# Performance work log

Hardware: AMD Instinct MI355X
Metric: run time of the kernel (lower is better)

## Reference

```python
import jax, jax.numpy as jnp
import numpy as np

B, T, H, D = 1, 2048, 32, 64
SCALE = 0.015625  # 1/64 = 1/head_size
DEG = 2


def setup_inputs() -> dict:
    key = jax.random.key(0)
    k1, k2, k3, k4 = jax.random.split(key, 4)
    q = jax.random.normal(k1, (B, T, H, D), dtype=jnp.float32)
    k = jax.random.normal(k2, (B, T, H, D), dtype=jnp.float32)
    v = jax.random.normal(k3, (B, T, H, D), dtype=jnp.float32)
    # log_G: per-token, per-head log decay (must be <= 0)
    g = -0.1 * jax.random.uniform(k4, (B, T, H), dtype=jnp.float32)
    return {"q": q, "k": k, "v": v, "g": g}


def reference(q, k, v, g):
    # q,k,v: [B,T,H,D]; g: [B,T,H] log-decay (log_G)
    # Power retention, deg=2, attention (quadratic) form for T <= switch_over_seq_len.
    g_cum = jnp.cumsum(g, axis=1)                         # [B,T,H]
    gc = jnp.transpose(g_cum, (0, 2, 1))                  # [B,H,T]
    # decay weight exp(gc[t]-gc[s]) for s<=t, 0 otherwise
    log_decay = gc[:, :, :, None] - gc[:, :, None, :]     # [B,H,T,S]
    causal = jnp.tril(jnp.ones((T, T), dtype=bool))
    decay = jnp.where(causal, jnp.exp(log_decay), 0.0)    # [B,H,T,S]
    qk = jnp.einsum("bthd,bshd->bhts", q, k) * SCALE      # [B,H,T,S]
    w = (qk ** DEG) * decay                               # nonneg scores, deg=2
    num = jnp.einsum("bhts,bshd->bthd", w, v)             # [B,T,H,D]
    denom = jnp.transpose(w.sum(-1), (0, 2, 1))           # [B,T,H]
    out = num / jnp.maximum(denom, 1.0)[..., None]
    return out
```

## Files before the change

### kernel.cpp

```cpp
#include <hip/hip_runtime.h>

#define T_DIM 2048
#define H_DIM 32
#define D_DIM 64
#define SCALE_F 0.015625f
#define NPAIR 32
#define TILE_STRIDE 2048

typedef unsigned short ushort;
typedef __attribute__((ext_vector_type(8))) short short8;
typedef __attribute__((ext_vector_type(16))) float f32x16;

__global__ __launch_bounds__(256)
void cumsum_g_kernel(const float* __restrict__ g, float* __restrict__ gc) {
    const int h = blockIdx.x;
    const int tid = threadIdx.x;
    const int PER = T_DIM / 256;

    __shared__ float sums[256];

    float loc[8];
    float run = 0.f;
    const int t0 = tid * PER;
    for (int i = 0; i < PER; ++i) {
        run += g[(size_t)(t0 + i) * H_DIM + h];
        loc[i] = run;
    }
    sums[tid] = run;
    __syncthreads();

    for (int off = 1; off < 256; off <<= 1) {
        float vv = (tid >= off) ? sums[tid - off] : 0.f;
        __syncthreads();
        sums[tid] += vv;
        __syncthreads();
    }
    float excl = (tid == 0) ? 0.f : sums[tid - 1];

    for (int i = 0; i < PER; ++i)
        gc[(size_t)h * T_DIM + t0 + i] = excl + loc[i];
}

__device__ __forceinline__ ushort f2bf(float x) {
    unsigned u = __float_as_uint(x);
    unsigned r = (u + 0x7fffu + ((u >> 16) & 1u)) >> 16;
    return (ushort)r;
}

__global__ __launch_bounds__(256)
void prep_kernel(const float* __restrict__ q, const float* __restrict__ k,
                 const float* __restrict__ v, const float* __restrict__ gc,
                 ushort* __restrict__ qfrag, ushort* __restrict__ kfrag,
                 ushort* __restrict__ vfrag) {
    __shared__ ushort qt_l[64 * 64];
    __shared__ ushort kt_l[64 * 64];

    const int tt  = blockIdx.x;
    const int h   = blockIdx.y;
    const int tid = threadIdx.x;

    {
        const int r    = tid >> 2;
        const int dseg = (tid & 3) * 16;
        const int t    = tt * 64 + r;
        const float gct = gc[(size_t)h * T_DIM + t];
        const float eq = SCALE_F * __expf(0.5f * gct);
        const float ek = __expf(-0.5f * gct);
        const float* qp = q + ((size_t)t * H_DIM + h) * 64 + dseg;
        const float* kp = k + ((size_t)t * H_DIM + h) * 64 + dseg;
        union { ushort u[16]; uint4 uu[2]; } oq, ok;
#pragma unroll
        for (int i = 0; i < 16; ++i) {
            oq.u[i] = f2bf(qp[i] * eq);
            ok.u[i] = f2bf(kp[i] * ek);
        }
        const int c0 = (tid & 3) * 2;
#pragma unroll
        for (int cc = 0; cc < 2; ++cc) {
            const int slot = (c0 + cc) ^ (r & 7);
            *reinterpret_cast<uint4*>(&qt_l[r * 64 + slot * 8]) = oq.uu[cc];
            *reinterpret_cast<uint4*>(&kt_l[r * 64 + slot * 8]) = ok.uu[cc];
        }
    }
    __syncthreads();

#pragma unroll
    for (int n = 0; n < 2; ++n) {
        const int ch   = tid + 256 * n;
        const int l31  = ch & 31;
        const int hi   = (ch >> 5) & 1;
        const int ks   = (ch >> 6) & 3;
        const int t32r = ch >> 8;
        const int row  = t32r * 32 + l31;
        const int slot = (2 * ks + hi) ^ (row & 7);
        uint4 qq = *reinterpret_cast<const uint4*>(&qt_l[row * 64 + slot * 8]);
        uint4 kk = *reinterpret_cast<const uint4*>(&kt_l[row * 64 + slot * 8]);
        const size_t base = ((size_t)h * 64 + tt * 2 + t32r) * TILE_STRIDE
                          + (size_t)(((ks * 2 + hi) * 32) + l31) * 8;
        *reinterpret_cast<uint4*>(qfrag + base) = qq;
        *reinterpret_cast<uint4*>(kfrag + base) = kk;
    }

#pragma unroll
    for (int n = 0; n < 2; ++n) {
        const int c9   = (tid >> 5) + 8 * n;
        const int l31  = tid & 31;
        const int hi   = c9 & 1;
        const int kh2  = (c9 >> 1) & 1;
        const int dblk = (c9 >> 2) & 1;
        const int s32r = c9 >> 3;
        const int tb = tt * 64 + s32r * 32 + kh2 * 16 + hi * 8;
        union { ushort u[8]; uint4 uu; } ov;
#pragma unroll
        for (int j = 0; j < 8; ++j)
            ov.u[j] = f2bf(v[((size_t)(tb + j) * H_DIM + h) * 64 + dblk * 32 + l31]);
        const size_t base = ((size_t)h * 64 + tt * 2 + s32r) * TILE_STRIDE
                          + (size_t)((((dblk * 2 + kh2) * 2 + hi) * 32) + l31) * 8;
        *reinterpret_cast<uint4*>(vfrag + base) = ov.uu;
    }
}

__device__ __forceinline__ short8 ld8(const ushort* p) {
    return *reinterpret_cast<const short8*>(p);
}

__device__ __forceinline__ unsigned cvt_pk_bf16(float lo, float hi) {
    unsigned r;
    asm("v_cvt_pk_bf16_f32 %0, %1, %2" : "=v"(r) : "v"(lo), "v"(hi));
    return r;
}

template<bool DIAG>
__device__ __forceinline__ void step32(
    const ushort* __restrict__ kb, const ushort* __restrict__ vb,
    int lofs, int hi, int l31,
    const short8 (&qr)[4], f32x16& o0, f32x16& o1, float& den)
{
    const short8 vf00 = ld8(vb + lofs);
    const short8 vf10 = ld8(vb + 512 + lofs);
    const short8 vf01 = ld8(vb + 1024 + lofs);
    const short8 vf11 = ld8(vb + 1536 + lofs);
    const short8 kf0 = ld8(kb + lofs);
    const short8 kf1 = ld8(kb + 512 + lofs);
    const short8 kf2 = ld8(kb + 1024 + lofs);
    const short8 kf3 = ld8(kb + 1536 + lofs);

    f32x16 c;
#pragma unroll
    for (int i = 0; i < 16; ++i) c[i] = 0.f;
    c = __builtin_amdgcn_mfma_f32_32x32x16_bf16(kf0, qr[0], c, 0, 0, 0);
    c = __builtin_amdgcn_mfma_f32_32x32x16_bf16(kf1, qr[1], c, 0, 0, 0);
    c = __builtin_amdgcn_mfma_f32_32x32x16_bf16(kf2, qr[2], c, 0, 0, 0);
    c = __builtin_amdgcn_mfma_f32_32x32x16_bf16(kf3, qr[3], c, 0, 0, 0);

    float w[16];
#pragma unroll
    for (int r = 0; r < 16; ++r) {
        float x = c[r];
        float ww = x * x;
        if (DIAG) {
            const int s_local = (r & 3) + 8 * (r >> 2) + 4 * hi;
            ww = (s_local <= l31) ? ww : 0.f;
        }
        w[r] = ww;
        den += ww;
    }

#pragma unroll
    for (int kh2 = 0; kh2 < 2; ++kh2) {
        const int b = 8 * kh2;
        unsigned p0 = cvt_pk_bf16(w[b + 0], w[b + 1]);
        unsigned p1 = cvt_pk_bf16(w[b + 2], w[b + 3]);
        unsigned p2 = cvt_pk_bf16(w[b + 4], w[b + 5]);
        unsigned p3 = cvt_pk_bf16(w[b + 6], w[b + 7]);
        asm("v_permlane32_swap_b32 %0, %1" : "+v"(p0), "+v"(p2));
        asm("v_permlane32_swap_b32 %0, %1" : "+v"(p1), "+v"(p3));
        union { unsigned u[4]; short8 s; } af;
        af.u[0] = p0; af.u[1] = p1; af.u[2] = p2; af.u[3] = p3;
        if (kh2 == 0) {
            o0 = __builtin_amdgcn_mfma_f32_32x32x16_bf16(af.s, vf00, o0, 0, 0, 0);
            o1 = __builtin_amdgcn_mfma_f32_32x32x16_bf16(af.s, vf01, o1, 0, 0, 0);
        } else {
            o0 = __builtin_amdgcn_mfma_f32_32x32x16_bf16(af.s, vf10, o0, 0, 0, 0);
            o1 = __builtin_amdgcn_mfma_f32_32x32x16_bf16(af.s, vf11, o1, 0, 0, 0);
        }
    }
}

__device__ __forceinline__ void process_subtile(
    int oo, int h, int w, int hi, int l31, int lofs,
    const ushort* __restrict__ qfrag, const ushort* __restrict__ kfrag,
    const ushort* __restrict__ vfrag, float* __restrict__ out,
    float* lds_o, float* lds_den)
{
    short8 qr[4];
    const ushort* qb = qfrag + ((size_t)h * 64 + oo) * TILE_STRIDE;
#pragma unroll
    for (int ks = 0; ks < 4; ++ks) qr[ks] = ld8(qb + ks * 512 + lofs);

    f32x16 o0, o1;
#pragma unroll
    for (int i = 0; i < 16; ++i) { o0[i] = 0.f; o1[i] = 0.f; }
    float den = 0.f;

    const ushort* kh_b = kfrag + (size_t)h * 64 * TILE_STRIDE;
    const ushort* vh_b = vfrag + (size_t)h * 64 * TILE_STRIDE;

    for (int st = w; st < oo; st += 4)
        step32<false>(kh_b + (size_t)st * TILE_STRIDE, vh_b + (size_t)st * TILE_STRIDE,
                      lofs, hi, l31, qr, o0, o1, den);
    if ((oo & 3) == w)
        step32<true>(kh_b + (size_t)oo * TILE_STRIDE, vh_b + (size_t)oo * TILE_STRIDE,
                     lofs, hi, l31, qr, o0, o1, den);

    den += __shfl_xor(den, 32);

    __syncthreads();
#pragma unroll
    for (int r = 0; r < 16; ++r) {
        const int row = (r & 3) + 8 * (r >> 2) + 4 * hi;
        lds_o[((w * 2 + 0) * 32 + row) * 32 + l31] = o0[r];
        lds_o[((w * 2 + 1) * 32 + row) * 32 + l31] = o1[r];
    }
    if (hi == 0) lds_den[w * 32 + l31] = den;
    __syncthreads();

    const float dtot = lds_den[l31] + lds_den[32 + l31] +
                       lds_den[64 + l31] + lds_den[96 + l31];
    const int t0 = oo * 32;
#pragma unroll
    for (int qq = 0; qq < 4; ++qq) {
        const int row = qq + 8 * w + 4 * hi;
        float s0 = 0.f, s1 = 0.f;
#pragma unroll
        for (int ww = 0; ww < 4; ++ww) {
            s0 += lds_o[((ww * 2 + 0) * 32 + row) * 32 + l31];
            s1 += lds_o[((ww * 2 + 1) * 32 + row) * 32 + l31];
        }
        const float dt = __shfl(dtot, row);
        const float inv = 1.f / fmaxf(dt, 1.f);
        float* op = out + ((size_t)(t0 + row) * H_DIM + h) * 64;
        op[l31]      = s0 * inv;
        op[32 + l31] = s1 * inv;
    }
}

__global__ __launch_bounds__(256, 4)
void retention_mfma_kernel(const ushort* __restrict__ qfrag,
                           const ushort* __restrict__ kfrag,
                           const ushort* __restrict__ vfrag,
                           float* __restrict__ out) {
    __shared__ float lds_o[4 * 2 * 32 * 32];
    __shared__ float lds_den[4 * 32];

    const int bid = blockIdx.x;
    const int p   = bid >> 5;
    const int h   = bid & 31;
    const int lane = threadIdx.x & 63;
    const int w    = threadIdx.x >> 6;
    const int hi   = lane >> 5;
    const int l31  = lane & 31;
    const int lofs = hi * 256 + l31 * 8;

    process_subtile(63 - p, h, w, hi, l31, lofs, qfrag, kfrag, vfrag, out, lds_o, lds_den);
    process_subtile(p,      h, w, hi, l31, lofs, qfrag, kfrag, vfrag, out, lds_o, lds_den);
}

extern "C" void kernel_launch(void* const* d_in, const int* in_sizes, int n_in,
                              void* d_out, int out_size, void* d_ws, size_t ws_size,
                              hipStream_t stream) {
    const float* q = (const float*)d_in[0];
    const float* k = (const float*)d_in[1];
    const float* v = (const float*)d_in[2];
    const float* g = (const float*)d_in[3];
    float* out = (float*)d_out;

    const size_t GC_BYTES = (size_t)H_DIM * T_DIM * sizeof(float);
    const size_t BF_ELEMS = (size_t)H_DIM * T_DIM * D_DIM;

    float* gc = (float*)d_ws;
    ushort* qfrag = (ushort*)((char*)d_ws + GC_BYTES);
    ushort* kfrag = qfrag + BF_ELEMS;
    ushort* vfrag = kfrag + BF_ELEMS;

    cumsum_g_kernel<<<H_DIM, 256, 0, stream>>>(g, gc);
    prep_kernel<<<dim3(T_DIM / 64, H_DIM), 256, 0, stream>>>(q, k, v, gc,
                                                             qfrag, kfrag, vfrag);
    retention_mfma_kernel<<<NPAIR * H_DIM, 256, 0, stream>>>(qfrag, kfrag, vfrag, out);
}
```

Before: 47.88 us.

## Process 64-row query tiles per block to reuse K/V fragment loads

```diff
diff --git a/kernel.cpp b/kernel.cpp
--- a/kernel.cpp
+++ b/kernel.cpp
@@ -4,7 +4,6 @@
 #define H_DIM 32
 #define D_DIM 64
 #define SCALE_F 0.015625f
-#define NPAIR 32
 #define TILE_STRIDE 2048
 
 typedef unsigned short ushort;
@@ -55,8 +54,8 @@
     __shared__ ushort qt_l[64 * 64];
     __shared__ ushort kt_l[64 * 64];
 
-    const int tt  = blockIdx.x;
-    const int h   = blockIdx.y;
+    const int h   = blockIdx.x;
+    const int tt  = blockIdx.y;
     const int tid = threadIdx.x;
 
     {
@@ -130,11 +129,25 @@
     return r;
 }
 
-template<bool DIAG>
-__device__ __forceinline__ void step32(
+__device__ __forceinline__ short8 pack_w(const float* w8) {
+    unsigned p0 = cvt_pk_bf16(w8[0], w8[1]);
+    unsigned p1 = cvt_pk_bf16(w8[2], w8[3]);
+    unsigned p2 = cvt_pk_bf16(w8[4], w8[5]);
+    unsigned p3 = cvt_pk_bf16(w8[6], w8[7]);
+    asm("v_permlane32_swap_b32 %0, %1" : "+v"(p0), "+v"(p2));
+    asm("v_permlane32_swap_b32 %0, %1" : "+v"(p1), "+v"(p3));
+    union { unsigned u[4]; short8 s; } af;
+    af.u[0] = p0; af.u[1] = p1; af.u[2] = p2; af.u[3] = p3;
+    return af.s;
+}
+
+template<int MODE>
+__device__ __forceinline__ void step64(
     const ushort* __restrict__ kb, const ushort* __restrict__ vb,
     int lofs, int hi, int l31,
-    const short8 (&qr)[4], f32x16& o0, f32x16& o1, float& den)
+    const short8 (&qrL)[4], const short8 (&qrH)[4],
+    f32x16& o00, f32x16& o01, f32x16& o10, f32x16& o11,
+    float& denL, float& denH)
 {
     const short8 vf00 = ld8(vb + lofs);
     const short8 vf10 = ld8(vb + 512 + lofs);
@@ -145,113 +158,145 @@
     const short8 kf2 = ld8(kb + 1024 + lofs);
     const short8 kf3 = ld8(kb + 1536 + lofs);
 
-    f32x16 c;
-#pragma unroll
-    for (int i = 0; i < 16; ++i) c[i] = 0.f;
-    c = __builtin_amdgcn_mfma_f32_32x32x16_bf16(kf0, qr[0], c, 0, 0, 0);
-    c = __builtin_amdgcn_mfma_f32_32x32x16_bf16(kf1, qr[1], c, 0, 0, 0);
-    c = __builtin_amdgcn_mfma_f32_32x32x16_bf16(kf2, qr[2], c, 0, 0, 0);
-    c = __builtin_amdgcn_mfma_f32_32x32x16_bf16(kf3, qr[3], c, 0, 0, 0);
-
-    float w[16];
+    f32x16 cH;
+#pragma unroll
+    for (int i = 0; i < 16; ++i) cH[i] = 0.f;
+    f32x16 cL = cH;
+
+    if (MODE <= 1) {
+        cL = __builtin_amdgcn_mfma_f32_32x32x16_bf16(kf0, qrL[0], cL, 0, 0, 0);
+        cH = __builtin_amdgcn_mfma_f32_32x32x16_bf16(kf0, qrH[0], cH, 0, 0, 0);
+        cL = __builtin_amdgcn_mfma_f32_32x32x16_bf16(kf1, qrL[1], cL, 0, 0, 0);
+        cH = __builtin_amdgcn_mfma_f32_32x32x16_bf16(kf1, qrH[1], cH, 0, 0, 0);
+        cL = __builtin_amdgcn_mfma_f32_32x32x16_bf16(kf2, qrL[2], cL, 0, 0, 0);
+        cH = __builtin_amdgcn_mfma_f32_32x32x16_bf16(kf2, qrH[2], cH, 0, 0, 0);
+        cL = __builtin_amdgcn_mfma_f32_32x32x16_bf16(kf3, qrL[3], cL, 0, 0, 0);
+        cH = __builtin_amdgcn_mfma_f32_32x32x16_bf16(kf3, qrH[3], cH, 0, 0, 0);
+    } else {
+        cH = __builtin_amdgcn_mfma_f32_32x32x16_bf16(kf0, qrH[0], cH, 0, 0, 0);
+        cH = __builtin_amdgcn_mfma_f32_32x32x16_bf16(kf1, qrH[1], cH, 0, 0, 0);
+        cH = __builtin_amdgcn_mfma_f32_32x32x16_bf16(kf2, qrH[2], cH, 0, 0, 0);
+        cH = __builtin_amdgcn_mfma_f32_32x32x16_bf16(kf3, qrH[3], cH, 0, 0, 0);
+    }
+
+    float wL[16], wH[16];
 #pragma unroll
     for (int r = 0; r < 16; ++r) {
-        float x = c[r];
-        float ww = x * x;
-        if (DIAG) {
-            const int s_local = (r & 3) + 8 * (r >> 2) + 4 * hi;
-            ww = (s_local <= l31) ? ww : 0.f;
+        const int s_local = (r & 3) + 8 * (r >> 2) + 4 * hi;
+        float xh = cH[r];
+        float wwh = xh * xh;
+        if (MODE == 2) wwh = (s_local <= l31) ? wwh : 0.f;
+        wH[r] = wwh;
+        denH += wwh;
+        if (MODE <= 1) {
+            float xl = cL[r];
+            float wwl = xl * xl;
+            if (MODE == 1) wwl = (s_local <= l31) ? wwl : 0.f;
+            wL[r] = wwl;
+            denL += wwl;
         }
-        w[r] = ww;
-        den += ww;
-    }
-
-#pragma unroll
-    for (int kh2 = 0; kh2 < 2; ++kh2) {
-        const int b = 8 * kh2;
-        unsigned p0 = cvt_pk_bf16(w[b + 0], w[b + 1]);
-        unsigned p1 = cvt_pk_bf16(w[b + 2], w[b + 3]);
-        unsigned p2 = cvt_pk_bf16(w[b + 4], w[b + 5]);
-        unsigned p3 = cvt_pk_bf16(w[b + 6], w[b + 7]);
-        asm("v_permlane32_swap_b32 %0, %1" : "+v"(p0), "+v"(p2));
-        asm("v_permlane32_swap_b32 %0, %1" : "+v"(p1), "+v"(p3));
-        union { unsigned u[4]; short8 s; } af;
-        af.u[0] = p0; af.u[1] = p1; af.u[2] = p2; af.u[3] = p3;
-        if (kh2 == 0) {
-            o0 = __builtin_amdgcn_mfma_f32_32x32x16_bf16(af.s, vf00, o0, 0, 0, 0);
-            o1 = __builtin_amdgcn_mfma_f32_32x32x16_bf16(af.s, vf01, o1, 0, 0, 0);
-        } else {
-            o0 = __builtin_amdgcn_mfma_f32_32x32x16_bf16(af.s, vf10, o0, 0, 0, 0);
-            o1 = __builtin_amdgcn_mfma_f32_32x32x16_bf16(af.s, vf11, o1, 0, 0, 0);
-        }
-    }
-}
-
-__device__ __forceinline__ void process_subtile(
-    int oo, int h, int w, int hi, int l31, int lofs,
+    }
+
+    if (MODE <= 1) {
+        const short8 a0 = pack_w(&wL[0]);
+        o00 = __builtin_amdgcn_mfma_f32_32x32x16_bf16(a0, vf00, o00, 0, 0, 0);
+        o01 = __builtin_amdgcn_mfma_f32_32x32x16_bf16(a0, vf01, o01, 0, 0, 0);
+        const short8 a1 = pack_w(&wL[8]);
+        o00 = __builtin_amdgcn_mfma_f32_32x32x16_bf16(a1, vf10, o00, 0, 0, 0);
+        o01 = __builtin_amdgcn_mfma_f32_32x32x16_bf16(a1, vf11, o01, 0, 0, 0);
+    }
+    {
+        const short8 a0 = pack_w(&wH[0]);
+        o10 = __builtin_amdgcn_mfma_f32_32x32x16_bf16(a0, vf00, o10, 0, 0, 0);
+        o11 = __builtin_amdgcn_mfma_f32_32x32x16_bf16(a0, vf01, o11, 0, 0, 0);
+        const short8 a1 = pack_w(&wH[8]);
+        o10 = __builtin_amdgcn_mfma_f32_32x32x16_bf16(a1, vf10, o10, 0, 0, 0);
+        o11 = __builtin_amdgcn_mfma_f32_32x32x16_bf16(a1, vf11, o11, 0, 0, 0);
+    }
+}
+
+__device__ __forceinline__ void epi_phase(
+    int thalf, const f32x16& od0, const f32x16& od1,
+    int t0, int h, int w, int hi, int l31,
+    float* __restrict__ out, float* lds_o, const float* lds_den)
+{
+    __syncthreads();
+#pragma unroll
+    for (int r = 0; r < 16; ++r) {
+        const int row = (r & 3) + 8 * (r >> 2) + 4 * hi;
+        lds_o[((w * 2 + 0) * 32 + row) * 32 + l31] = od0[r];
+        lds_o[((w * 2 + 1) * 32 + row) * 32 + l31] = od1[r];
+    }
+    __syncthreads();
+#pragma unroll
+    for (int rr = 0; rr < 8; ++rr) {
+        const int row = 8 * w + rr;
+        const float s = lds_o[((0 + hi) * 32 + row) * 32 + l31]
+                      + lds_o[((2 + hi) * 32 + row) * 32 + l31]
+                      + lds_o[((4 + hi) * 32 + row) * 32 + l31]
+                      + lds_o[((6 + hi) * 32 + row) * 32 + l31];
+        const float dt = lds_den[(0 + thalf) * 32 + row]
+                       + lds_den[(2 + thalf) * 32 + row]
+                       + lds_den[(4 + thalf) * 32 + row]
+                       + lds_den[(6 + thalf) * 32 + row];
+        const float inv = 1.f / fmaxf(dt, 1.f);
+        out[((size_t)(t0 + thalf * 32 + row) * H_DIM + h) * 64 + hi * 32 + l31]
+            = s * inv;
+    }
+}
+
+__device__ __forceinline__ void process_tile64(
+    int tt, int h, int w, int hi, int l31, int lofs,
     const ushort* __restrict__ qfrag, const ushort* __restrict__ kfrag,
     const ushort* __restrict__ vfrag, float* __restrict__ out,
     float* lds_o, float* lds_den)
 {
-    short8 qr[4];
-    const ushort* qb = qfrag + ((size_t)h * 64 + oo) * TILE_STRIDE;
-#pragma unroll
-    for (int ks = 0; ks < 4; ++ks) qr[ks] = ld8(qb + ks * 512 + lofs);
-
-    f32x16 o0, o1;
-#pragma unroll
-    for (int i = 0; i < 16; ++i) { o0[i] = 0.f; o1[i] = 0.f; }
-    float den = 0.f;
+    short8 qrL[4], qrH[4];
+    const ushort* qb = qfrag + ((size_t)h * 64 + 2 * tt) * TILE_STRIDE;
+#pragma unroll
+    for (int ks = 0; ks < 4; ++ks) {
+        qrL[ks] = ld8(qb + ks * 512 + lofs);
+        qrH[ks] = ld8(qb + TILE_STRIDE + ks * 512 + lofs);
+    }
+
+    f32x16 o00, o01, o10, o11;
+#pragma unroll
+    for (int i = 0; i < 16; ++i) { o00[i] = 0.f; o01[i] = 0.f; o10[i] = 0.f; o11[i] = 0.f; }
+    float denL = 0.f, denH = 0.f;
 
     const ushort* kh_b = kfrag + (size_t)h * 64 * TILE_STRIDE;
     const ushort* vh_b = vfrag + (size_t)h * 64 * TILE_STRIDE;
-
-    for (int st = w; st < oo; st += 4)
-        step32<false>(kh_b + (size_t)st * TILE_STRIDE, vh_b + (size_t)st * TILE_STRIDE,
-                      lofs, hi, l31, qr, o0, o1, den);
-    if ((oo & 3) == w)
-        step32<true>(kh_b + (size_t)oo * TILE_STRIDE, vh_b + (size_t)oo * TILE_STRIDE,
-                     lofs, hi, l31, qr, o0, o1, den);
-
-    den += __shfl_xor(den, 32);
-
-    __syncthreads();
-#pragma unroll
-    for (int r = 0; r < 16; ++r) {
-        const int row = (r & 3) + 8 * (r >> 2) + 4 * hi;
-        lds_o[((w * 2 + 0) * 32 + row) * 32 + l31] = o0[r];
-        lds_o[((w * 2 + 1) * 32 + row) * 32 + l31] = o1[r];
-    }
-    if (hi == 0) lds_den[w * 32 + l31] = den;
-    __syncthreads();
-
-    const float dtot = lds_den[l31] + lds_den[32 + l31] +
-                       lds_den[64 + l31] + lds_den[96 + l31];
-    const int t0 = oo * 32;
-#pragma unroll
-    for (int qq = 0; qq < 4; ++qq) {
-        const int row = qq + 8 * w + 4 * hi;
-        float s0 = 0.f, s1 = 0.f;
-#pragma unroll
-        for (int ww = 0; ww < 4; ++ww) {
-            s0 += lds_o[((ww * 2 + 0) * 32 + row) * 32 + l31];
-            s1 += lds_o[((ww * 2 + 1) * 32 + row) * 32 + l31];
-        }
-        const float dt = __shfl(dtot, row);
-        const float inv = 1.f / fmaxf(dt, 1.f);
-        float* op = out + ((size_t)(t0 + row) * H_DIM + h) * 64;
-        op[l31]      = s0 * inv;
-        op[32 + l31] = s1 * inv;
-    }
-}
-
-__global__ __launch_bounds__(256, 4)
+    const int dlo = 2 * tt;
+
+    for (int st = w; st < dlo; st += 4)
+        step64<0>(kh_b + (size_t)st * TILE_STRIDE, vh_b + (size_t)st * TILE_STRIDE,
+                  lofs, hi, l31, qrL, qrH, o00, o01, o10, o11, denL, denH);
+    if ((dlo & 3) == w)
+        step64<1>(kh_b + (size_t)dlo * TILE_STRIDE, vh_b + (size_t)dlo * TILE_STRIDE,
+                  lofs, hi, l31, qrL, qrH, o00, o01, o10, o11, denL, denH);
+    if (((dlo + 1) & 3) == w)
+        step64<2>(kh_b + (size_t)(dlo + 1) * TILE_STRIDE, vh_b + (size_t)(dlo + 1) * TILE_STRIDE,
+                  lofs, hi, l31, qrL, qrH, o00, o01, o10, o11, denL, denH);
+
+    denL += __shfl_xor(denL, 32);
+    denH += __shfl_xor(denH, 32);
+    if (hi == 0) {
+        lds_den[(w * 2 + 0) * 32 + l31] = denL;
+        lds_den[(w * 2 + 1) * 32 + l31] = denH;
+    }
+
+    const int t0 = tt * 64;
+    epi_phase(0, o00, o01, t0, h, w, hi, l31, out, lds_o, lds_den);
+    epi_phase(1, o10, o11, t0, h, w, hi, l31, out, lds_o, lds_den);
+}
+
+__global__ __launch_bounds__(256, 2)
 void retention_mfma_kernel(const ushort* __restrict__ qfrag,
                            const ushort* __restrict__ kfrag,
                            const ushort* __restrict__ vfrag,
                            float* __restrict__ out) {
     __shared__ float lds_o[4 * 2 * 32 * 32];
-    __shared__ float lds_den[4 * 32];
+    __shared__ float lds_den[4 * 2 * 32];
 
     const int bid = blockIdx.x;
     const int p   = bid >> 5;
@@ -262,8 +307,8 @@
     const int l31  = lane & 31;
     const int lofs = hi * 256 + l31 * 8;
 
-    process_subtile(63 - p, h, w, hi, l31, lofs, qfrag, kfrag, vfrag, out, lds_o, lds_den);
-    process_subtile(p,      h, w, hi, l31, lofs, qfrag, kfrag, vfrag, out, lds_o, lds_den);
+    process_tile64(31 - p, h, w, hi, l31, lofs, qfrag, kfrag, vfrag, out, lds_o, lds_den);
+    process_tile64(p,      h, w, hi, l31, lofs, qfrag, kfrag, vfrag, out, lds_o, lds_den);
 }
 
 extern "C" void kernel_launch(void* const* d_in, const int* in_sizes, int n_in,
@@ -284,7 +329,7 @@
     ushort* vfrag = kfrag + BF_ELEMS;
 
     cumsum_g_kernel<<<H_DIM, 256, 0, stream>>>(g, gc);
-    prep_kernel<<<dim3(T_DIM / 64, H_DIM), 256, 0, stream>>>(q, k, v, gc,
+    prep_kernel<<<dim3(H_DIM, T_DIM / 64), 256, 0, stream>>>(q, k, v, gc,
                                                              qfrag, kfrag, vfrag);
-    retention_mfma_kernel<<<NPAIR * H_DIM, 256, 0, stream>>>(qfrag, kfrag, vfrag, out);
-}
+    retention_mfma_kernel<<<16 * H_DIM, 256, 0, stream>>>(qfrag, kfrag, vfrag, out);
+}
```

Result: faster. 45.47 us (-5.0%).

## Stage K/V tiles through LDS with double-buffered async loads over 64-row tile pairs

Applied to the files above, without the earlier changes.

```diff
diff --git a/kernel.cpp b/kernel.cpp
--- a/kernel.cpp
+++ b/kernel.cpp
@@ -4,12 +4,14 @@
 #define H_DIM 32
 #define D_DIM 64
 #define SCALE_F 0.015625f
-#define NPAIR 32
 #define TILE_STRIDE 2048
 
 typedef unsigned short ushort;
 typedef __attribute__((ext_vector_type(8))) short short8;
 typedef __attribute__((ext_vector_type(16))) float f32x16;
+typedef __attribute__((ext_vector_type(2))) float f32x2;
+
+#define MFMA32(A, B, C) __builtin_amdgcn_mfma_f32_32x32x16_bf16((A), (B), (C), 0, 0, 0)
 
 __global__ __launch_bounds__(256)
 void cumsum_g_kernel(const float* __restrict__ g, float* __restrict__ gc) {
@@ -55,8 +57,8 @@
     __shared__ ushort qt_l[64 * 64];
     __shared__ ushort kt_l[64 * 64];
 
-    const int tt  = blockIdx.x;
-    const int h   = blockIdx.y;
+    const int h   = blockIdx.x;
+    const int tt  = blockIdx.y;
     const int tid = threadIdx.x;
 
     {
@@ -130,140 +132,205 @@
     return r;
 }
 
-template<bool DIAG>
-__device__ __forceinline__ void step32(
-    const ushort* __restrict__ kb, const ushort* __restrict__ vb,
+__device__ __forceinline__ short8 pack_w2(const f32x2* w2) {
+    unsigned p0 = cvt_pk_bf16(w2[0][0], w2[0][1]);
+    unsigned p1 = cvt_pk_bf16(w2[1][0], w2[1][1]);
+    unsigned p2 = cvt_pk_bf16(w2[2][0], w2[2][1]);
+    unsigned p3 = cvt_pk_bf16(w2[3][0], w2[3][1]);
+    asm("v_permlane32_swap_b32 %0, %1" : "+v"(p0), "+v"(p2));
+    asm("v_permlane32_swap_b32 %0, %1" : "+v"(p1), "+v"(p3));
+    union { unsigned u[4]; short8 s; } af;
+    af.u[0] = p0; af.u[1] = p1; af.u[2] = p2; af.u[3] = p3;
+    return af.s;
+}
+
+__device__ __forceinline__ void gll16(const void* g, void* l) {
+    __builtin_amdgcn_global_load_lds(
+        (const __attribute__((address_space(1))) unsigned int*)g,
+        (__attribute__((address_space(3))) unsigned int*)l, 16, 0, 0);
+}
+
+__device__ __forceinline__ void stage16k(ushort* ldst, const char* ksrc,
+                                         const char* vsrc, int tid) {
+    char* lb = (char*)ldst + (tid >> 6) * 1024;
+    const int lo = tid * 16;
+    gll16(ksrc + lo,        lb);
+    gll16(ksrc + 4096 + lo, lb + 4096);
+    gll16(vsrc + lo,        lb + 8192);
+    gll16(vsrc + 4096 + lo, lb + 12288);
+}
+
+template<int MODE>
+__device__ __forceinline__ void unit32(
+    const ushort* ldsK, const ushort* ldsV,
     int lofs, int hi, int l31,
-    const short8 (&qr)[4], f32x16& o0, f32x16& o1, float& den)
+    const short8 (&qr)[4], f32x16& o0, f32x16& o1, f32x2& den2)
 {
-    const short8 vf00 = ld8(vb + lofs);
-    const short8 vf10 = ld8(vb + 512 + lofs);
-    const short8 vf01 = ld8(vb + 1024 + lofs);
-    const short8 vf11 = ld8(vb + 1536 + lofs);
-    const short8 kf0 = ld8(kb + lofs);
-    const short8 kf1 = ld8(kb + 512 + lofs);
-    const short8 kf2 = ld8(kb + 1024 + lofs);
-    const short8 kf3 = ld8(kb + 1536 + lofs);
+    const short8 kf0 = ld8(ldsK + lofs);
+    const short8 kf1 = ld8(ldsK + 512 + lofs);
+    const short8 kf2 = ld8(ldsK + 1024 + lofs);
+    const short8 kf3 = ld8(ldsK + 1536 + lofs);
+    const short8 vf0 = ld8(ldsV + lofs);
+    const short8 vf1 = ld8(ldsV + 512 + lofs);
+    const short8 vf2 = ld8(ldsV + 1024 + lofs);
+    const short8 vf3 = ld8(ldsV + 1536 + lofs);
 
     f32x16 c;
 #pragma unroll
     for (int i = 0; i < 16; ++i) c[i] = 0.f;
-    c = __builtin_amdgcn_mfma_f32_32x32x16_bf16(kf0, qr[0], c, 0, 0, 0);
-    c = __builtin_amdgcn_mfma_f32_32x32x16_bf16(kf1, qr[1], c, 0, 0, 0);
-    c = __builtin_amdgcn_mfma_f32_32x32x16_bf16(kf2, qr[2], c, 0, 0, 0);
-    c = __builtin_amdgcn_mfma_f32_32x32x16_bf16(kf3, qr[3], c, 0, 0, 0);
-
-    float w[16];
-#pragma unroll
-    for (int r = 0; r < 16; ++r) {
-        float x = c[r];
-        float ww = x * x;
-        if (DIAG) {
-            const int s_local = (r & 3) + 8 * (r >> 2) + 4 * hi;
-            ww = (s_local <= l31) ? ww : 0.f;
-        }
-        w[r] = ww;
-        den += ww;
-    }
-
-#pragma unroll
-    for (int kh2 = 0; kh2 < 2; ++kh2) {
-        const int b = 8 * kh2;
-        unsigned p0 = cvt_pk_bf16(w[b + 0], w[b + 1]);
-        unsigned p1 = cvt_pk_bf16(w[b + 2], w[b + 3]);
-        unsigned p2 = cvt_pk_bf16(w[b + 4], w[b + 5]);
-        unsigned p3 = cvt_pk_bf16(w[b + 6], w[b + 7]);
-        asm("v_permlane32_swap_b32 %0, %1" : "+v"(p0), "+v"(p2));
-        asm("v_permlane32_swap_b32 %0, %1" : "+v"(p1), "+v"(p3));
-        union { unsigned u[4]; short8 s; } af;
-        af.u[0] = p0; af.u[1] = p1; af.u[2] = p2; af.u[3] = p3;
-        if (kh2 == 0) {
-            o0 = __builtin_amdgcn_mfma_f32_32x32x16_bf16(af.s, vf00, o0, 0, 0, 0);
-            o1 = __builtin_amdgcn_mfma_f32_32x32x16_bf16(af.s, vf01, o1, 0, 0, 0);
-        } else {
-            o0 = __builtin_amdgcn_mfma_f32_32x32x16_bf16(af.s, vf10, o0, 0, 0, 0);
-            o1 = __builtin_amdgcn_mfma_f32_32x32x16_bf16(af.s, vf11, o1, 0, 0, 0);
-        }
-    }
-}
-
-__device__ __forceinline__ void process_subtile(
-    int oo, int h, int w, int hi, int l31, int lofs,
-    const ushort* __restrict__ qfrag, const ushort* __restrict__ kfrag,
-    const ushort* __restrict__ vfrag, float* __restrict__ out,
-    float* lds_o, float* lds_den)
-{
-    short8 qr[4];
-    const ushort* qb = qfrag + ((size_t)h * 64 + oo) * TILE_STRIDE;
-#pragma unroll
-    for (int ks = 0; ks < 4; ++ks) qr[ks] = ld8(qb + ks * 512 + lofs);
-
-    f32x16 o0, o1;
-#pragma unroll
-    for (int i = 0; i < 16; ++i) { o0[i] = 0.f; o1[i] = 0.f; }
-    float den = 0.f;
-
-    const ushort* kh_b = kfrag + (size_t)h * 64 * TILE_STRIDE;
-    const ushort* vh_b = vfrag + (size_t)h * 64 * TILE_STRIDE;
-
-    for (int st = w; st < oo; st += 4)
-        step32<false>(kh_b + (size_t)st * TILE_STRIDE, vh_b + (size_t)st * TILE_STRIDE,
-                      lofs, hi, l31, qr, o0, o1, den);
-    if ((oo & 3) == w)
-        step32<true>(kh_b + (size_t)oo * TILE_STRIDE, vh_b + (size_t)oo * TILE_STRIDE,
-                     lofs, hi, l31, qr, o0, o1, den);
-
-    den += __shfl_xor(den, 32);
-
-    __syncthreads();
-#pragma unroll
-    for (int r = 0; r < 16; ++r) {
-        const int row = (r & 3) + 8 * (r >> 2) + 4 * hi;
-        lds_o[((w * 2 + 0) * 32 + row) * 32 + l31] = o0[r];
-        lds_o[((w * 2 + 1) * 32 + row) * 32 + l31] = o1[r];
-    }
-    if (hi == 0) lds_den[w * 32 + l31] = den;
-    __syncthreads();
-
-    const float dtot = lds_den[l31] + lds_den[32 + l31] +
-                       lds_den[64 + l31] + lds_den[96 + l31];
-    const int t0 = oo * 32;
-#pragma unroll
-    for (int qq = 0; qq < 4; ++qq) {
-        const int row = qq + 8 * w + 4 * hi;
-        float s0 = 0.f, s1 = 0.f;
-#pragma unroll
-        for (int ww = 0; ww < 4; ++ww) {
-            s0 += lds_o[((ww * 2 + 0) * 32 + row) * 32 + l31];
-            s1 += lds_o[((ww * 2 + 1) * 32 + row) * 32 + l31];
-        }
-        const float dt = __shfl(dtot, row);
-        const float inv = 1.f / fmaxf(dt, 1.f);
-        float* op = out + ((size_t)(t0 + row) * H_DIM + h) * 64;
-        op[l31]      = s0 * inv;
-        op[32 + l31] = s1 * inv;
-    }
-}
-
-__global__ __launch_bounds__(256, 4)
+    c = MFMA32(kf0, qr[0], c);
+    c = MFMA32(kf1, qr[1], c);
+    c = MFMA32(kf2, qr[2], c);
+    c = MFMA32(kf3, qr[3], c);
+
+    f32x2 w2[8];
+#pragma unroll
+    for (int i = 0; i < 8; ++i) {
+        const int r0 = 2 * i;
+        f32x2 x; x[0] = c[r0]; x[1] = c[r0 + 1];
+        f32x2 ww = x * x;
+        if (MODE == 1) {
+            const int sl0 = (r0 & 3) + 8 * (r0 >> 2) + 4 * hi;
+            ww[0] = (sl0 <= l31) ? ww[0] : 0.f;
+            ww[1] = (sl0 + 1 <= l31) ? ww[1] : 0.f;
+        }
+        w2[i] = ww;
+        den2 += ww;
+    }
+    const short8 a0 = pack_w2(&w2[0]);
+    o0 = MFMA32(a0, vf0, o0);
+    o1 = MFMA32(a0, vf2, o1);
+    const short8 a1 = pack_w2(&w2[4]);
+    o0 = MFMA32(a1, vf1, o0);
+    o1 = MFMA32(a1, vf3, o1);
+}
+
+__global__ __launch_bounds__(256, 2)
 void retention_mfma_kernel(const ushort* __restrict__ qfrag,
                            const ushort* __restrict__ kfrag,
                            const ushort* __restrict__ vfrag,
                            float* __restrict__ out) {
-    __shared__ float lds_o[4 * 2 * 32 * 32];
-    __shared__ float lds_den[4 * 32];
+    __shared__ ushort buf[2][8192];
+    __shared__ float lds_red[2][2][32][32];
+    __shared__ float lds_den[2][32];
 
     const int bid = blockIdx.x;
     const int p   = bid >> 5;
     const int h   = bid & 31;
-    const int lane = threadIdx.x & 63;
-    const int w    = threadIdx.x >> 6;
-    const int hi   = lane >> 5;
-    const int l31  = lane & 31;
+    const int ht  = 31 - p;
+    const int tid = threadIdx.x;
+    const int w   = tid >> 6;
+    const int lane = tid & 63;
+    const int hi  = lane >> 5;
+    const int l31 = lane & 31;
     const int lofs = hi * 256 + l31 * 8;
 
-    process_subtile(63 - p, h, w, hi, l31, lofs, qfrag, kfrag, vfrag, out, lds_o, lds_den);
-    process_subtile(p,      h, w, hi, l31, lofs, qfrag, kfrag, vfrag, out, lds_o, lds_den);
+    short8 qrA[4], qrB[4];
+    {
+        const int prim_t32 = (w < 2) ? (ht * 2 + w) : (p * 2 + (w - 2));
+        const ushort* qa = qfrag + ((size_t)h * 64 + prim_t32) * TILE_STRIDE;
+#pragma unroll
+        for (int ks = 0; ks < 4; ++ks) qrA[ks] = ld8(qa + ks * 512 + lofs);
+        if (w >= 2) {
+            const int sec_t32 = ht * 2 + (w - 2);
+            const ushort* qb = qfrag + ((size_t)h * 64 + sec_t32) * TILE_STRIDE;
+#pragma unroll
+            for (int ks = 0; ks < 4; ++ks) qrB[ks] = ld8(qb + ks * 512 + lofs);
+        }
+    }
+
+    f32x16 a0, a1, b0, b1;
+#pragma unroll
+    for (int i = 0; i < 16; ++i) { a0[i] = 0.f; a1[i] = 0.f; b0[i] = 0.f; b1[i] = 0.f; }
+    f32x2 dA, dB;
+    dA[0] = 0.f; dA[1] = 0.f; dB[0] = 0.f; dB[1] = 0.f;
+
+    const char* kgb = (const char*)(kfrag + (size_t)h * 64 * TILE_STRIDE);
+    const char* vgb = (const char*)(vfrag + (size_t)h * 64 * TILE_STRIDE);
+
+    stage16k(buf[0], kgb, vgb, tid);
+    __syncthreads();
+
+    int cur = 0;
+    for (int J = 0; J <= ht; ++J) {
+        if (J < ht)
+            stage16k(buf[cur ^ 1], kgb + (size_t)(J + 1) * 8192,
+                     vgb + (size_t)(J + 1) * 8192, tid);
+
+        const ushort* K0 = &buf[cur][0];
+        const ushort* K1 = &buf[cur][2048];
+        const ushort* V0 = &buf[cur][4096];
+        const ushort* V1 = &buf[cur][6144];
+
+        if (J < p) {
+            unit32<0>(K0, V0, lofs, hi, l31, qrA, a0, a1, dA);
+            unit32<0>(K1, V1, lofs, hi, l31, qrA, a0, a1, dA);
+        } else if (J == p) {
+            if (w < 2) {
+                unit32<0>(K0, V0, lofs, hi, l31, qrA, a0, a1, dA);
+                unit32<0>(K1, V1, lofs, hi, l31, qrA, a0, a1, dA);
+            } else if (w == 2) {
+                unit32<1>(K0, V0, lofs, hi, l31, qrA, a0, a1, dA);
+            } else {
+                unit32<0>(K0, V0, lofs, hi, l31, qrA, a0, a1, dA);
+                unit32<1>(K1, V1, lofs, hi, l31, qrA, a0, a1, dA);
+            }
+        } else if (J < ht) {
+            if (w < 2) unit32<0>(K0, V0, lofs, hi, l31, qrA, a0, a1, dA);
+            else       unit32<0>(K1, V1, lofs, hi, l31, qrB, b0, b1, dB);
+        } else {
+            if (w == 0)      unit32<1>(K0, V0, lofs, hi, l31, qrA, a0, a1, dA);
+            else if (w == 1) unit32<0>(K0, V0, lofs, hi, l31, qrA, a0, a1, dA);
+            else if (w == 3) unit32<1>(K1, V1, lofs, hi, l31, qrB, b0, b1, dB);
+        }
+
+        __syncthreads();
+        cur ^= 1;
+    }
+
+    float denA = dA[0] + dA[1];
+    denA += __shfl_xor(denA, 32);
+    float denB = dB[0] + dB[1];
+    denB += __shfl_xor(denB, 32);
+
+    if (w >= 2) {
+        const int ww = w - 2;
+#pragma unroll
+        for (int r = 0; r < 16; ++r) {
+            const int row = (r & 3) + 8 * (r >> 2) + 4 * hi;
+            lds_red[ww][0][row][l31] = b0[r];
+            lds_red[ww][1][row][l31] = b1[r];
+        }
+        if (hi == 0) lds_den[ww][l31] = denB;
+    }
+    __syncthreads();
+
+    if (w < 2) {
+        const float dlane = denA + lds_den[w][l31];
+#pragma unroll
+        for (int r = 0; r < 16; ++r) {
+            const int row = (r & 3) + 8 * (r >> 2) + 4 * hi;
+            const float s0 = a0[r] + lds_red[w][0][row][l31];
+            const float s1 = a1[r] + lds_red[w][1][row][l31];
+            const float dt = __shfl(dlane, row);
+            const float inv = 1.f / fmaxf(dt, 1.f);
+            const int t = ht * 64 + w * 32 + row;
+            float* op = out + ((size_t)t * H_DIM + h) * 64;
+            op[l31]      = s0 * inv;
+            op[32 + l31] = s1 * inv;
+        }
+    } else {
+#pragma unroll
+        for (int r = 0; r < 16; ++r) {
+            const int row = (r & 3) + 8 * (r >> 2) + 4 * hi;
+            const float dt = __shfl(denA, row);
+            const float inv = 1.f / fmaxf(dt, 1.f);
+            const int t = p * 64 + (w - 2) * 32 + row;
+            float* op = out + ((size_t)t * H_DIM + h) * 64;
+            op[l31]      = a0[r] * inv;
+            op[32 + l31] = a1[r] * inv;
+        }
+    }
 }
 
 extern "C" void kernel_launch(void* const* d_in, const int* in_sizes, int n_in,
@@ -284,7 +351,7 @@
     ushort* vfrag = kfrag + BF_ELEMS;
 
     cumsum_g_kernel<<<H_DIM, 256, 0, stream>>>(g, gc);
-    prep_kernel<<<dim3(T_DIM / 64, H_DIM), 256, 0, stream>>>(q, k, v, gc,
+    prep_kernel<<<dim3(H_DIM, T_DIM / 64), 256, 0, stream>>>(q, k, v, gc,
                                                              qfrag, kfrag, vfrag);
-    retention_mfma_kernel<<<NPAIR * H_DIM, 256, 0, stream>>>(qfrag, kfrag, vfrag, out);
-}
+    retention_mfma_kernel<<<16 * H_DIM, 256, 0, stream>>>(qfrag, kfrag, vfrag, out);
+}
```

New measurement: 54.58 us. 14.0% more time.
